# Kernel tuning notes

Measured on AMD Instinct MI355X. Metric: run time of the kernel, lower is better.

## Reference

```python
import jax, jax.numpy as jnp
import numpy as np


def _conv(x, w):
    # stride-2, pad-1, 3x3 conv, NCHW activations, HWIO kernel
    return jax.lax.conv_general_dilated(
        x, w, (2, 2), [(1, 1), (1, 1)],
        dimension_numbers=('NCHW', 'HWIO', 'NCHW'))


def setup_inputs() -> dict:
    key = jax.random.key(0)
    ks = iter(jax.random.split(key, 40))
    def rn(shape, scale=1.0):
        return jax.random.normal(next(ks), shape, jnp.float32) * scale
    d = {}
    d['img'] = rn((64, 3, 128, 128))
    d['qst'] = rn((64, 128))
    d['conv_w0'] = rn((3, 3, 3, 24), 1.0 / np.sqrt(3 * 9))
    for i in (1, 2, 3):
        d['conv_w%d' % i] = rn((3, 3, 24, 24), 1.0 / np.sqrt(24 * 9))
    for i in range(4):
        d['bn_s%d' % i] = jax.random.uniform(next(ks), (24,), jnp.float32, 0.5, 1.5)
        d['bn_b%d' % i] = rn((24,), 0.1)
    d['g_w1'] = rn((180, 256), 1.0 / np.sqrt(180))
    d['g_b1'] = rn((256,), 0.01)
    for i in (2, 3, 4):
        d['g_w%d' % i] = rn((256, 256), 1.0 / np.sqrt(256))
        d['g_b%d' % i] = rn((256,), 0.01)
    d['f_w1'] = rn((256, 256), 1.0 / np.sqrt(256))
    d['f_b1'] = rn((256,), 0.01)
    d['f_w2'] = rn((256, 256), 1.0 / np.sqrt(256))
    d['f_b2'] = rn((256,), 0.01)
    d['cls_w'] = rn((256, 32), 1.0 / np.sqrt(256))
    d['cls_b'] = rn((32,), 0.01)
    return d


def reference(img, qst, conv_w0, conv_w1, conv_w2, conv_w3,
              bn_s0, bn_b0, bn_s1, bn_b1, bn_s2, bn_b2, bn_s3, bn_b3,
              g_w1, g_b1, g_w2, g_b2, g_w3, g_b3, g_w4, g_b4,
              f_w1, f_b1, f_w2, f_b2, cls_w, cls_b):
    x = img
    for w, s, b in ((conv_w0, bn_s0, bn_b0), (conv_w1, bn_s1, bn_b1),
                    (conv_w2, bn_s2, bn_b2), (conv_w3, bn_s3, bn_b3)):
        x = jax.nn.relu(_conv(x, w) * s[None, :, None, None] + b[None, :, None, None])
    N, C, H, W = x.shape  # [64, 24, 8, 8]
    # positional encoding: coords_x, coords_y in [-1,1]
    cx, cy = jnp.meshgrid(jnp.linspace(-1.0, 1.0, W), jnp.linspace(-1.0, 1.0, H))
    pos = jnp.broadcast_to(jnp.stack([cx, cy])[None], (N, 2, H, W)).astype(x.dtype)
    x = jnp.concatenate([x, pos], axis=1)              # [N, C+2, H, W]
    Cf = C + 2
    x = x.transpose(0, 2, 3, 1).reshape(N, H * W, Cf)  # [N, HW, 26]
    # RN_G first linear decomposed over concat([x_i, x_j, qst]) so the huge
    # [N, HW, HW, 2C+q] concat tensor is never materialized (same math).
    W1a, W1b, W1c = g_w1[:Cf], g_w1[Cf:2 * Cf], g_w1[2 * Cf:]
    hi = x @ W1a                      # [N, HW, 256]
    hj = x @ W1b                      # [N, HW, 256]
    hq = qst @ W1c + g_b1             # [N, 256]
    h = jax.nn.relu(hi[:, :, None, :] + hj[:, None, :, :] + hq[:, None, None, :])  # [N,HW,HW,256]
    h = jax.nn.relu(h @ g_w2 + g_b2)
    h = jax.nn.relu(h @ g_w3 + g_b3)
    h = jax.nn.relu(h @ g_w4 + g_b4)
    s = h.sum(axis=(1, 2))            # sum over all HW*HW pairs -> [N, 256]
    # RN_F (dropout is identity in eval mode)
    y = jax.nn.relu(s @ f_w1 + f_b1)
    y = jax.nn.relu(y @ f_w2 + f_b2)
    return jax.nn.log_softmax(y @ cls_w + cls_b, axis=1)
```

## Files before the change

### kernel.cpp

```cpp
#include <hip/hip_runtime.h>
#include <hip/hip_bf16.h>
#include <math.h>

typedef __bf16 bf16x8 __attribute__((ext_vector_type(8)));
typedef __bf16 bf16x4 __attribute__((ext_vector_type(4)));
typedef float  f32x4  __attribute__((ext_vector_type(4)));

#define LH 264

__device__ __host__ inline int fperm(int p) {
  return (p & 0xC0) | ((p & 0x0C) << 2) | ((p >> 2) & 0x0C) | (p & 3);
}

__global__ __launch_bounds__(256) void k1(const float* __restrict__ img, const float* __restrict__ w0,
    const float* __restrict__ bs0, const float* __restrict__ bb0,
    const float* __restrict__ g2, const float* __restrict__ g3, const float* __restrict__ g4,
    const float* __restrict__ gw1, const float* __restrict__ gb1, const float* __restrict__ qst,
    float* __restrict__ c0, __bf16* __restrict__ Wt, float* __restrict__ hq,
    float* __restrict__ sbuf) {
  __shared__ __align__(16) float smem[8224];
  const int blk = blockIdx.x, t = threadIdx.x;

  if (blk < 512) {
    float* wl = smem;
    for (int i = t; i < 648; i += 256) wl[i] = w0[i];
    __syncthreads();
    const int H = 128, W = 128, OH = 64, OW = 64;
    int idx = blk * 256 + t;
    int oxh = idx & 31; int tt = idx >> 5; int oy = tt & 63; int n = tt >> 6;
    int ox0 = oxh * 2;
    float acc0[24], acc1[24];
#pragma unroll
    for (int co = 0; co < 24; ++co) { acc0[co] = 0.f; acc1[co] = 0.f; }
    for (int ci = 0; ci < 3; ++ci) {
      const float* xp = img + (size_t)(n * 3 + ci) * H * W;
      float in[3][7];
#pragma unroll
      for (int ky = 0; ky < 3; ++ky) {
        int iy = 2 * oy + ky - 1;
        bool yok = (iy >= 0) && (iy < H);
        const float* row = xp + (size_t)iy * W;
#pragma unroll
        for (int u = 0; u < 7; ++u) {
          int ix = 2 * ox0 - 1 + u;
          in[ky][u] = (yok && ix >= 0 && ix < W) ? row[ix] : 0.f;
        }
      }
#pragma unroll
      for (int ky = 0; ky < 3; ++ky)
#pragma unroll
        for (int kx = 0; kx < 3; ++kx) {
          const float* wp = &wl[((ky * 3 + kx) * 3 + ci) * 24];
          float v0 = in[ky][kx], v1 = in[ky][kx + 2];
#pragma unroll
          for (int co = 0; co < 24; ++co) {
            float wv = wp[co];
            acc0[co] += v0 * wv;
            acc1[co] += v1 * wv;
          }
        }
    }
    float* yp = c0 + (size_t)n * 24 * OH * OW + (size_t)oy * OW + ox0;
#pragma unroll
    for (int co = 0; co < 24; ++co) {
      float s = bs0[co], b = bb0[co];
      yp[(size_t)co * OH * OW]     = fmaxf(acc0[co] * s + b, 0.f);
      yp[(size_t)co * OH * OW + 1] = fmaxf(acc1[co] * s + b, 0.f);
    }
  } else if (blk < 536) {
    float* tile = smem;
    const int lb = blk - 512;
    const int l = lb >> 3, ks = lb & 7;
    const float* src = (l == 0) ? g2 : (l == 1) ? g3 : g4;
    for (int kk = 0; kk < 32; ++kk) tile[kk * 257 + t] = src[(ks * 32 + kk) * 256 + t];
    __syncthreads();
    const int q = t & 3, nb = t >> 2;
    __bf16* out = Wt + (size_t)(l * 8 + ks) * 8192;
#pragma unroll
    for (int i = 0; i < 4; ++i) {
      int nn = i * 64 + nb;
      int fsel = (l < 2) ? fperm(nn) : nn;
      bf16x8 v;
#pragma unroll
      for (int j = 0; j < 8; ++j) v[j] = (__bf16)tile[(q * 8 + j) * 257 + fsel];
      *(bf16x8*)&out[nn * 32 + q * 8] = v;
    }
  } else {
    float* qs = smem;
    const int n = blk - 536;
    sbuf[n * 256 + t] = 0.f;
    if (t < 128) qs[t] = qst[n * 128 + t];
    __syncthreads();
    float a = gb1[t];
    for (int c = 0; c < 128; ++c) a += qs[c] * gw1[(52 + c) * 256 + t];
    hq[n * 256 + t] = a;
  }
}

__global__ __launch_bounds__(256) void conv1_k(const float* __restrict__ x, const float* __restrict__ w,
                                               const float* __restrict__ sc, const float* __restrict__ bi,
                                               float* __restrict__ y) {
  const int H = 64, W = 64, OH = 32, OW = 32;
  __shared__ float wl[2592];
  const int half = blockIdx.x & 1, sb = blockIdx.x >> 1;
  for (int i = threadIdx.x; i < 2592; i += 256) {
    int co = i % 12, rest = i / 12;
    wl[i] = w[rest * 24 + half * 12 + co];
  }
  __syncthreads();

  int idx = sb * 256 + threadIdx.x;
  int ox = idx & 31, oy = (idx >> 5) & 31, n = idx >> 10;

  float acc[12];
#pragma unroll
  for (int co = 0; co < 12; ++co) acc[co] = 0.f;

  for (int ci = 0; ci < 24; ++ci) {
    const float* xp = x + (size_t)(n * 24 + ci) * H * W;
#pragma unroll
    for (int ky = 0; ky < 3; ++ky) {
      int iy = 2 * oy + ky - 1;
      if (iy < 0 || iy >= H) continue;
      const float* row = xp + (size_t)iy * W;
      float in[3];
#pragma unroll
      for (int u = 0; u < 3; ++u) {
        int ix = 2 * ox - 1 + u;
        in[u] = (ix >= 0 && ix < W) ? row[ix] : 0.f;
      }
#pragma unroll
      for (int kx = 0; kx < 3; ++kx) {
        const float* wp = &wl[((ky * 3 + kx) * 24 + ci) * 12];
        float v = in[kx];
#pragma unroll
        for (int co = 0; co < 12; ++co) acc[co] += v * wp[co];
      }
    }
  }
  float* yp = y + (size_t)(n * 24 + half * 12) * OH * OW + (size_t)oy * OW + ox;
#pragma unroll
  for (int co = 0; co < 12; ++co) {
    int cog = half * 12 + co;
    yp[(size_t)co * OH * OW] = fmaxf(acc[co] * sc[cog] + bi[cog], 0.f);
  }
}

__global__ __launch_bounds__(256) void chain2_k(const float* __restrict__ c1,
    const float* __restrict__ w2, const float* __restrict__ bs2, const float* __restrict__ bb2,
    const float* __restrict__ w3, const float* __restrict__ bs3, const float* __restrict__ bb3,
    const float* __restrict__ gw1, float* __restrict__ hi, float* __restrict__ hj) {
  __shared__ float sw[5184];
  __shared__ float s2[6144];
  __shared__ float s3[1536];
  const int n = blockIdx.x, t = threadIdx.x;
  for (int i = t; i < 5184; i += 256) sw[i] = w2[i];
  __syncthreads();
  {
    int ox = t & 15, oy = t >> 4;
    float acc[24];
#pragma unroll
    for (int co = 0; co < 24; ++co) acc[co] = 0.f;
    for (int ci = 0; ci < 24; ++ci) {
      const float* xp = c1 + (size_t)(n * 24 + ci) * 1024;
#pragma unroll
      for (int ky = 0; ky < 3; ++ky) {
        int iy = 2 * oy + ky - 1;
        if (iy < 0 || iy >= 32) continue;
#pragma unroll
        for (int kx = 0; kx < 3; ++kx) {
          int ix = 2 * ox + kx - 1;
          if (ix < 0 || ix >= 32) continue;
          float v = xp[iy * 32 + ix];
          const float* wp = &sw[((ky * 3 + kx) * 24 + ci) * 24];
#pragma unroll
          for (int co = 0; co < 24; ++co) acc[co] += v * wp[co];
        }
      }
    }
#pragma unroll
    for (int co = 0; co < 24; ++co)
      s2[co * 256 + t] = fmaxf(acc[co] * bs2[co] + bb2[co], 0.f);
  }
  __syncthreads();
  for (int i = t; i < 5184; i += 256) sw[i] = w3[i];
  __syncthreads();
  {
    const int pos = t & 63, cog = t >> 6;
    const int oy = pos >> 3, ox = pos & 7;
    float acc[6];
#pragma unroll
    for (int u = 0; u < 6; ++u) acc[u] = 0.f;
    for (int ci = 0; ci < 24; ++ci) {
      const float* cp = &s2[ci * 256];
#pragma unroll
      for (int ky = 0; ky < 3; ++ky) {
        int iy = 2 * oy + ky - 1;
        if (iy < 0 || iy >= 16) continue;
#pragma unroll
        for (int kx = 0; kx < 3; ++kx) {
          int ix = 2 * ox + kx - 1;
          if (ix < 0 || ix >= 16) continue;
          float v = cp[iy * 16 + ix];
          const float* wp = &sw[((ky * 3 + kx) * 24 + ci) * 24 + cog * 6];
#pragma unroll
          for (int u = 0; u < 6; ++u) acc[u] += v * wp[u];
        }
      }
    }
#pragma unroll
    for (int u = 0; u < 6; ++u) {
      int co = cog * 6 + u;
      s3[co * 64 + pos] = fmaxf(acc[u] * bs3[co] + bb3[co], 0.f);
    }
  }
  float wa[26], wb[26];
#pragma unroll
  for (int c = 0; c < 26; ++c) {
    wa[c] = gw1[c * 256 + t];
    wb[c] = gw1[(26 + c) * 256 + t];
  }
  __syncthreads();
  for (int p = 0; p < 64; ++p) {
    float a = 0.f, b = 0.f;
#pragma unroll
    for (int c = 0; c < 24; ++c) {
      float v = s3[c * 64 + p];
      a += v * wa[c];
      b += v * wb[c];
    }
    float cx = -1.f + (2.f / 7.f) * (float)(p & 7);
    float cy = -1.f + (2.f / 7.f) * (float)(p >> 3);
    a += cx * wa[24] + cy * wa[25];
    b += cx * wb[24] + cy * wb[25];
    hi[(size_t)(n * 64 + p) * 256 + t] = a;
    hj[(size_t)(n * 64 + p) * 256 + t] = b;
  }
}

__global__ __launch_bounds__(256, 2)
void g_fused(const float* __restrict__ hi, const float* __restrict__ hj,
             const float* __restrict__ hq, const __bf16* __restrict__ Wt,
             const float* __restrict__ b2, const float* __restrict__ b3,
             const float* __restrict__ b4, float* __restrict__ s_out) {
  const int blk = blockIdx.x;
  const int n = blk >> 5, ib = blk & 31;
  const int tid = threadIdx.x;
  const int wave = tid >> 6, lane = tid & 63;
  const int q = lane >> 4, lr = lane & 15;

  __shared__ __align__(16) __bf16 Hs[128 * LH];

  const int half = lane >> 5, m = lane & 31;
  const int cb = m * 8;
  float4 hqA = *(const float4*)(hq + (size_t)n * 256 + cb);
  float4 hqB = *(const float4*)(hq + (size_t)n * 256 + cb + 4);
  float4 hiA = *(const float4*)(hi + (size_t)(n * 64 + ib * 2 + half) * 256 + cb);
  float4 hiB = *(const float4*)(hi + (size_t)(n * 64 + ib * 2 + half) * 256 + cb + 4);
  float hh[8];
  hh[0] = hiA.x + hqA.x; hh[1] = hiA.y + hqA.y; hh[2] = hiA.z + hqA.z; hh[3] = hiA.w + hqA.w;
  hh[4] = hiB.x + hqB.x; hh[5] = hiB.y + hqB.y; hh[6] = hiB.z + hqB.z; hh[7] = hiB.w + hqB.w;

  float bias2[4];
#pragma unroll
  for (int c = 0; c < 4; ++c) bias2[c] = b4[wave * 64 + lr + c * 16];

  const float* hjb = hj + (size_t)n * 64 * 256;
#pragma unroll
  for (int it = 0; it < 16; ++it) {
    int j = it * 4 + wave;
    float4 va = *(const float4*)(hjb + j * 256 + cb);
    float4 vb = *(const float4*)(hjb + j * 256 + cb + 4);
    bf16x8 o;
    o[0] = (__bf16)fmaxf(va.x + hh[0], 0.f);
    o[1] = (__bf16)fmaxf(va.y + hh[1], 0.f);
    o[2] = (__bf16)fmaxf(va.z + hh[2], 0.f);
    o[3] = (__bf16)fmaxf(va.w + hh[3], 0.f);
    o[4] = (__bf16)fmaxf(vb.x + hh[4], 0.f);
    o[5] = (__bf16)fmaxf(vb.y + hh[5], 0.f);
    o[6] = (__bf16)fmaxf(vb.z + hh[6], 0.f);
    o[7] = (__bf16)fmaxf(vb.w + hh[7], 0.f);
    *(bf16x8*)&Hs[(size_t)(half * 64 + j) * LH + cb] = o;
  }
  __syncthreads();

  const __bf16* Bp = Wt + (size_t)wave * 2048 + lr * 32 + q * 8;
  const int colv = wave * 64 + q * 16;

  for (int l = 0; l < 2; ++l) {
    const __bf16* Bl = Bp + (size_t)l * 65536;
    const float* bb = (l == 0) ? b2 : b3;
    f32x4 bv[4];
#pragma unroll
    for (int c = 0; c < 4; ++c)
      bv[c] = *(const f32x4*)(bb + colv + c * 4);

    f32x4 acc[8][4];
#pragma unroll
    for (int r = 0; r < 8; ++r)
#pragma unroll
      for (int c = 0; c < 4; ++c) acc[r][c] = (f32x4){0.f, 0.f, 0.f, 0.f};

    bf16x8 bnxt[4];
#pragma unroll
    for (int c = 0; c < 4; ++c) bnxt[c] = *(const bf16x8*)&Bl[c * 512];
#pragma unroll
    for (int ks = 0; ks < 8; ++ks) {
      bf16x8 bcur[4];
#pragma unroll
      for (int c = 0; c < 4; ++c) bcur[c] = bnxt[c];
      if (ks < 7) {
#pragma unroll
        for (int c = 0; c < 4; ++c) bnxt[c] = *(const bf16x8*)&Bl[(ks + 1) * 8192 + c * 512];
      }
      bf16x8 a[8];
#pragma unroll
      for (int r = 0; r < 8; ++r)
        a[r] = *(const bf16x8*)&Hs[(size_t)(r * 16 + lr) * LH + ks * 32 + q * 8];
      __builtin_amdgcn_s_setprio(1);
#pragma unroll
      for (int r = 0; r < 8; ++r)
#pragma unroll
        for (int c = 0; c < 4; ++c)
          acc[r][c] = __builtin_amdgcn_mfma_f32_16x16x32_bf16(bcur[c], a[r], acc[r][c], 0, 0, 0);
      __builtin_amdgcn_s_setprio(0);
    }

    __syncthreads();
#pragma unroll
    for (int r = 0; r < 8; ++r) {
      bf16x8 oA, oB;
#pragma unroll
      for (int c = 0; c < 2; ++c)
#pragma unroll
        for (int reg = 0; reg < 4; ++reg)
          oA[c * 4 + reg] = (__bf16)fmaxf(acc[r][c][reg] + bv[c][reg], 0.f);
#pragma unroll
      for (int c = 2; c < 4; ++c)
#pragma unroll
        for (int reg = 0; reg < 4; ++reg)
          oB[(c - 2) * 4 + reg] = (__bf16)fmaxf(acc[r][c][reg] + bv[c][reg], 0.f);
      __bf16* wp = &Hs[(size_t)(r * 16 + lr) * LH + colv];
      *(bf16x8*)wp = oA;
      *(bf16x8*)(wp + 8) = oB;
    }
    __syncthreads();
  }

  {
    const __bf16* Bl = Bp + (size_t)2 * 65536;
    f32x4 acc[8][4];
#pragma unroll
    for (int r = 0; r < 8; ++r)
#pragma unroll
      for (int c = 0; c < 4; ++c) acc[r][c] = (f32x4){0.f, 0.f, 0.f, 0.f};

    bf16x8 bnxt[4];
#pragma unroll
    for (int c = 0; c < 4; ++c) bnxt[c] = *(const bf16x8*)&Bl[c * 512];
#pragma unroll
    for (int ks = 0; ks < 8; ++ks) {
      bf16x8 bcur[4];
#pragma unroll
      for (int c = 0; c < 4; ++c) bcur[c] = bnxt[c];
      if (ks < 7) {
#pragma unroll
        for (int c = 0; c < 4; ++c) bnxt[c] = *(const bf16x8*)&Bl[(ks + 1) * 8192 + c * 512];
      }
      bf16x8 a[8];
#pragma unroll
      for (int r = 0; r < 8; ++r)
        a[r] = *(const bf16x8*)&Hs[(size_t)(r * 16 + lr) * LH + ks * 32 + q * 8];
      __builtin_amdgcn_s_setprio(1);
#pragma unroll
      for (int r = 0; r < 8; ++r)
#pragma unroll
        for (int c = 0; c < 4; ++c)
          acc[r][c] = __builtin_amdgcn_mfma_f32_16x16x32_bf16(a[r], bcur[c], acc[r][c], 0, 0, 0);
      __builtin_amdgcn_s_setprio(0);
    }

#pragma unroll
    for (int c = 0; c < 4; ++c) {
      float cs = 0.f;
#pragma unroll
      for (int r = 0; r < 8; ++r)
#pragma unroll
        for (int reg = 0; reg < 4; ++reg)
          cs += fmaxf(acc[r][c][reg] + bias2[c], 0.f);
      cs += __shfl_xor(cs, 16);
      cs += __shfl_xor(cs, 32);
      if (q == 0) atomicAdd(&s_out[n * 256 + wave * 64 + lr + c * 16], cs);
    }
  }
}

__global__ void f_net(const float* __restrict__ s, const float* __restrict__ fw1,
                      const float* __restrict__ fb1, const float* __restrict__ fw2,
                      const float* __restrict__ fb2, const float* __restrict__ cw,
                      const float* __restrict__ cb, float* __restrict__ out) {
  int n = blockIdx.x, t = threadIdx.x;
  __shared__ float buf[256], buf2[256], zs[32];
  buf[t] = s[n * 256 + t];
  __syncthreads();
  float a0 = 0.f, a1 = 0.f, a2 = 0.f, a3 = 0.f;
  for (int c = 0; c < 256; c += 4) {
    a0 += buf[c]     * fw1[c * 256 + t];
    a1 += buf[c + 1] * fw1[(c + 1) * 256 + t];
    a2 += buf[c + 2] * fw1[(c + 2) * 256 + t];
    a3 += buf[c + 3] * fw1[(c + 3) * 256 + t];
  }
  float a = fmaxf(fb1[t] + ((a0 + a1) + (a2 + a3)), 0.f);
  buf2[t] = a;
  __syncthreads();
  float y0 = 0.f, y1 = 0.f, y2 = 0.f, y3 = 0.f;
  for (int c = 0; c < 256; c += 4) {
    y0 += buf2[c]     * fw2[c * 256 + t];
    y1 += buf2[c + 1] * fw2[(c + 1) * 256 + t];
    y2 += buf2[c + 2] * fw2[(c + 2) * 256 + t];
    y3 += buf2[c + 3] * fw2[(c + 3) * 256 + t];
  }
  float y = fmaxf(fb2[t] + ((y0 + y1) + (y2 + y3)), 0.f);
  __syncthreads();
  buf[t] = y;
  __syncthreads();
  float z = 0.f;
  if (t < 32) {
    float z0 = 0.f, z1 = 0.f, z2 = 0.f, z3 = 0.f;
    for (int c = 0; c < 256; c += 4) {
      z0 += buf[c]     * cw[c * 32 + t];
      z1 += buf[c + 1] * cw[(c + 1) * 32 + t];
      z2 += buf[c + 2] * cw[(c + 2) * 32 + t];
      z3 += buf[c + 3] * cw[(c + 3) * 32 + t];
    }
    z = cb[t] + ((z0 + z1) + (z2 + z3));
    zs[t] = z;
  }
  __syncthreads();
  if (t < 32) {
    float mx = -1e30f;
    for (int c = 0; c < 32; ++c) mx = fmaxf(mx, zs[c]);
    float se = 0.f;
    for (int c = 0; c < 32; ++c) se += expf(zs[c] - mx);
    out[n * 32 + t] = z - mx - logf(se);
  }
}

extern "C" void kernel_launch(void* const* d_in, const int* in_sizes, int n_in,
                              void* d_out, int out_size, void* d_ws, size_t ws_size,
                              hipStream_t stream) {
  const float* img  = (const float*)d_in[0];
  const float* qst  = (const float*)d_in[1];
  const float* w0   = (const float*)d_in[2];
  const float* w1   = (const float*)d_in[3];
  const float* w2   = (const float*)d_in[4];
  const float* w3   = (const float*)d_in[5];
  const float* bs0  = (const float*)d_in[6];
  const float* bb0  = (const float*)d_in[7];
  const float* bs1  = (const float*)d_in[8];
  const float* bb1  = (const float*)d_in[9];
  const float* bs2  = (const float*)d_in[10];
  const float* bb2  = (const float*)d_in[11];
  const float* bs3  = (const float*)d_in[12];
  const float* bb3  = (const float*)d_in[13];
  const float* gw1  = (const float*)d_in[14];
  const float* gb1  = (const float*)d_in[15];
  const float* gw2  = (const float*)d_in[16];
  const float* gb2  = (const float*)d_in[17];
  const float* gw3  = (const float*)d_in[18];
  const float* gb3  = (const float*)d_in[19];
  const float* gw4  = (const float*)d_in[20];
  const float* gb4  = (const float*)d_in[21];
  const float* fw1  = (const float*)d_in[22];
  const float* fb1  = (const float*)d_in[23];
  const float* fw2  = (const float*)d_in[24];
  const float* fb2  = (const float*)d_in[25];
  const float* cw   = (const float*)d_in[26];
  const float* cb   = (const float*)d_in[27];

  char* ws = (char*)d_ws;
  float* c0 = (float*)(ws + 0);
  float* c1 = (float*)(ws + 25165824);
  __bf16* Wt  = (__bf16*)(ws + 31457280);
  float*  hqb = (float*)(ws + 31850496);
  float*  sbuf = (float*)(ws + 31916032);
  float*  hi  = (float*)(ws + 0);
  float*  hj  = (float*)(ws + 4194304);

  k1<<<600, 256, 0, stream>>>(img, w0, bs0, bb0, gw2, gw3, gw4, gw1, gb1, qst,
                              c0, Wt, hqb, sbuf);
  conv1_k<<<512, 256, 0, stream>>>(c0, w1, bs1, bb1, c1);
  chain2_k<<<64, 256, 0, stream>>>(c1, w2, bs2, bb2, w3, bs3, bb3, gw1, hi, hj);
  g_fused<<<2048, 256, 0, stream>>>(hi, hj, hqb, Wt, gb2, gb3, gb4, sbuf);
  f_net<<<64, 256, 0, stream>>>(sbuf, fw1, fb1, fw2, fb2, cw, cb, (float*)d_out);
}
```

Baseline: 307.9 us.

## Register-block conv1 outputs and split chain2 conv work across two blocks per image

conv1 now computes two adjacent output columns per thread, sharing a 7-wide input row window, and launches half as many blocks. chain2 is split into two blocks per image: each computes the conv2 rows its half of conv3 needs (with one overlapping halo row) and then half of the hi/hj positions. This doubles parallelism in the previously 64-block chain2 stage at the cost of some redundant conv2 work. conv0 also skips out-of-range rows early. The risk is fewer conv1 blocks and more registers per thread lowering occupancy.

```diff
diff --git a/kernel.cpp b/kernel.cpp
--- a/kernel.cpp
+++ b/kernel.cpp
@@ -34,24 +34,22 @@
     for (int co = 0; co < 24; ++co) { acc0[co] = 0.f; acc1[co] = 0.f; }
     for (int ci = 0; ci < 3; ++ci) {
       const float* xp = img + (size_t)(n * 3 + ci) * H * W;
-      float in[3][7];
 #pragma unroll
       for (int ky = 0; ky < 3; ++ky) {
         int iy = 2 * oy + ky - 1;
-        bool yok = (iy >= 0) && (iy < H);
+        if (iy < 0 || iy >= H) continue;
         const float* row = xp + (size_t)iy * W;
+        int ixb = 2 * ox0 - 1;
+        float in[7];
 #pragma unroll
         for (int u = 0; u < 7; ++u) {
-          int ix = 2 * ox0 - 1 + u;
-          in[ky][u] = (yok && ix >= 0 && ix < W) ? row[ix] : 0.f;
+          int ix = ixb + u;
+          in[u] = (ix >= 0 && ix < W) ? row[ix] : 0.f;
         }
-      }
-#pragma unroll
-      for (int ky = 0; ky < 3; ++ky)
 #pragma unroll
         for (int kx = 0; kx < 3; ++kx) {
           const float* wp = &wl[((ky * 3 + kx) * 3 + ci) * 24];
-          float v0 = in[ky][kx], v1 = in[ky][kx + 2];
+          float v0 = in[kx], v1 = in[kx + 2];
 #pragma unroll
           for (int co = 0; co < 24; ++co) {
             float wv = wp[co];
@@ -59,6 +57,7 @@
             acc1[co] += v1 * wv;
           }
         }
+      }
     }
     float* yp = c0 + (size_t)n * 24 * OH * OW + (size_t)oy * OW + ox0;
 #pragma unroll
@@ -110,11 +109,12 @@
   __syncthreads();
 
   int idx = sb * 256 + threadIdx.x;
-  int ox = idx & 31, oy = (idx >> 5) & 31, n = idx >> 10;
-
-  float acc[12];
-#pragma unroll
-  for (int co = 0; co < 12; ++co) acc[co] = 0.f;
+  int oxh = idx & 15; int tt = idx >> 4; int oy = tt & 31; int n = tt >> 5;
+  int ox0 = oxh * 2;
+
+  float acc0[12], acc1[12];
+#pragma unroll
+  for (int co = 0; co < 12; ++co) { acc0[co] = 0.f; acc1[co] = 0.f; }
 
   for (int ci = 0; ci < 24; ++ci) {
     const float* xp = x + (size_t)(n * 24 + ci) * H * W;
@@ -123,26 +123,33 @@
       int iy = 2 * oy + ky - 1;
       if (iy < 0 || iy >= H) continue;
       const float* row = xp + (size_t)iy * W;
-      float in[3];
-#pragma unroll
-      for (int u = 0; u < 3; ++u) {
-        int ix = 2 * ox - 1 + u;
+      int ixb = 2 * ox0 - 1;
+      float in[7];
+#pragma unroll
+      for (int u = 0; u < 7; ++u) {
+        int ix = ixb + u;
         in[u] = (ix >= 0 && ix < W) ? row[ix] : 0.f;
       }
 #pragma unroll
       for (int kx = 0; kx < 3; ++kx) {
         const float* wp = &wl[((ky * 3 + kx) * 24 + ci) * 12];
-        float v = in[kx];
-#pragma unroll
-        for (int co = 0; co < 12; ++co) acc[co] += v * wp[co];
-      }
-    }
-  }
-  float* yp = y + (size_t)(n * 24 + half * 12) * OH * OW + (size_t)oy * OW + ox;
+        float v0 = in[kx], v1 = in[kx + 2];
+#pragma unroll
+        for (int co = 0; co < 12; ++co) {
+          float wv = wp[co];
+          acc0[co] += v0 * wv;
+          acc1[co] += v1 * wv;
+        }
+      }
+    }
+  }
+  float* yp = y + (size_t)n * 24 * OH * OW + (size_t)(half * 12) * OH * OW + (size_t)oy * OW + ox0;
 #pragma unroll
   for (int co = 0; co < 12; ++co) {
     int cog = half * 12 + co;
-    yp[(size_t)co * OH * OW] = fmaxf(acc[co] * sc[cog] + bi[cog], 0.f);
+    float s = sc[cog], b = bi[cog];
+    yp[(size_t)co * OH * OW]     = fmaxf(acc0[co] * s + b, 0.f);
+    yp[(size_t)co * OH * OW + 1] = fmaxf(acc1[co] * s + b, 0.f);
   }
 }
 
@@ -151,13 +158,18 @@
     const float* __restrict__ w3, const float* __restrict__ bs3, const float* __restrict__ bb3,
     const float* __restrict__ gw1, float* __restrict__ hi, float* __restrict__ hj) {
   __shared__ float sw[5184];
-  __shared__ float s2[6144];
-  __shared__ float s3[1536];
-  const int n = blockIdx.x, t = threadIdx.x;
+  __shared__ float s2l[24 * 144];
+  __shared__ float s3l[24 * 32];
+  const int b = blockIdx.x, t = threadIdx.x;
+  const int n = b >> 1, h = b & 1;
+  const int row0 = (h == 0) ? 0 : 7;
+  const int nrows = (h == 0) ? 8 : 9;
+
   for (int i = t; i < 5184; i += 256) sw[i] = w2[i];
   __syncthreads();
-  {
-    int ox = t & 15, oy = t >> 4;
+  if (t < nrows * 16) {
+    int gr = row0 + (t >> 4);
+    int gx = t & 15;
     float acc[24];
 #pragma unroll
     for (int co = 0; co < 24; ++co) acc[co] = 0.f;
@@ -165,11 +177,11 @@
       const float* xp = c1 + (size_t)(n * 24 + ci) * 1024;
 #pragma unroll
       for (int ky = 0; ky < 3; ++ky) {
-        int iy = 2 * oy + ky - 1;
+        int iy = 2 * gr + ky - 1;
         if (iy < 0 || iy >= 32) continue;
 #pragma unroll
         for (int kx = 0; kx < 3; ++kx) {
-          int ix = 2 * ox + kx - 1;
+          int ix = 2 * gx + kx - 1;
           if (ix < 0 || ix >= 32) continue;
           float v = xp[iy * 32 + ix];
           const float* wp = &sw[((ky * 3 + kx) * 24 + ci) * 24];
@@ -180,38 +192,39 @@
     }
 #pragma unroll
     for (int co = 0; co < 24; ++co)
-      s2[co * 256 + t] = fmaxf(acc[co] * bs2[co] + bb2[co], 0.f);
+      s2l[co * 144 + t] = fmaxf(acc[co] * bs2[co] + bb2[co], 0.f);
   }
   __syncthreads();
   for (int i = t; i < 5184; i += 256) sw[i] = w3[i];
   __syncthreads();
   {
-    const int pos = t & 63, cog = t >> 6;
-    const int oy = pos >> 3, ox = pos & 7;
-    float acc[6];
-#pragma unroll
-    for (int u = 0; u < 6; ++u) acc[u] = 0.f;
+    const int pos = t & 31, cog = t >> 5;
+    const int oy3 = 4 * h + (pos >> 3), ox3 = pos & 7;
+    float acc[3];
+#pragma unroll
+    for (int u = 0; u < 3; ++u) acc[u] = 0.f;
     for (int ci = 0; ci < 24; ++ci) {
-      const float* cp = &s2[ci * 256];
+      const float* cp = &s2l[ci * 144];
 #pragma unroll
       for (int ky = 0; ky < 3; ++ky) {
-        int iy = 2 * oy + ky - 1;
-        if (iy < 0 || iy >= 16) continue;
+        int gy2 = 2 * oy3 + ky - 1;
+        if (gy2 < 0 || gy2 >= 16) continue;
+        int ly = gy2 - row0;
 #pragma unroll
         for (int kx = 0; kx < 3; ++kx) {
-          int ix = 2 * ox + kx - 1;
+          int ix = 2 * ox3 + kx - 1;
           if (ix < 0 || ix >= 16) continue;
-          float v = cp[iy * 16 + ix];
-          const float* wp = &sw[((ky * 3 + kx) * 24 + ci) * 24 + cog * 6];
-#pragma unroll
-          for (int u = 0; u < 6; ++u) acc[u] += v * wp[u];
+          float v = cp[ly * 16 + ix];
+          const float* wp = &sw[((ky * 3 + kx) * 24 + ci) * 24 + cog * 3];
+#pragma unroll
+          for (int u = 0; u < 3; ++u) acc[u] += v * wp[u];
         }
       }
     }
 #pragma unroll
-    for (int u = 0; u < 6; ++u) {
-      int co = cog * 6 + u;
-      s3[co * 64 + pos] = fmaxf(acc[u] * bs3[co] + bb3[co], 0.f);
+    for (int u = 0; u < 3; ++u) {
+      int co = cog * 3 + u;
+      s3l[co * 32 + pos] = fmaxf(acc[u] * bs3[co] + bb3[co], 0.f);
     }
   }
   float wa[26], wb[26];
@@ -221,20 +234,21 @@
     wb[c] = gw1[(26 + c) * 256 + t];
   }
   __syncthreads();
-  for (int p = 0; p < 64; ++p) {
-    float a = 0.f, b = 0.f;
+  for (int pl = 0; pl < 32; ++pl) {
+    int p = 32 * h + pl;
+    float a = 0.f, bv = 0.f;
 #pragma unroll
     for (int c = 0; c < 24; ++c) {
-      float v = s3[c * 64 + p];
+      float v = s3l[c * 32 + pl];
       a += v * wa[c];
-      b += v * wb[c];
+      bv += v * wb[c];
     }
     float cx = -1.f + (2.f / 7.f) * (float)(p & 7);
     float cy = -1.f + (2.f / 7.f) * (float)(p >> 3);
     a += cx * wa[24] + cy * wa[25];
-    b += cx * wb[24] + cy * wb[25];
+    bv += cx * wb[24] + cy * wb[25];
     hi[(size_t)(n * 64 + p) * 256 + t] = a;
-    hj[(size_t)(n * 64 + p) * 256 + t] = b;
+    hj[(size_t)(n * 64 + p) * 256 + t] = bv;
   }
 }
 
@@ -489,8 +503,8 @@
 
   k1<<<600, 256, 0, stream>>>(img, w0, bs0, bb0, gw2, gw3, gw4, gw1, gb1, qst,
                               c0, Wt, hqb, sbuf);
-  conv1_k<<<512, 256, 0, stream>>>(c0, w1, bs1, bb1, c1);
-  chain2_k<<<64, 256, 0, stream>>>(c1, w2, bs2, bb2, w3, bs3, bb3, gw1, hi, hj);
+  conv1_k<<<256, 256, 0, stream>>>(c0, w1, bs1, bb1, c1);
+  chain2_k<<<128, 256, 0, stream>>>(c1, w2, bs2, bb2, w3, bs3, bb3, gw1, hi, hj);
   g_fused<<<2048, 256, 0, stream>>>(hi, hj, hqb, Wt, gb2, gb3, gb4, sbuf);
   f_net<<<64, 256, 0, stream>>>(sbuf, fw1, fb1, fw2, fb2, cw, cb, (float*)d_out);
 }
```

After: 299.1 us (median of 2 runs). -2.9%, faster.
